# Performance work log

Hardware: AMD Instinct MI355X
Metric: run time of the kernel (lower is better)

Reference implementation:

```python
import jax, jax.numpy as jnp
import numpy as np

ASSET_DIM = 2048
NUM_LATENTS = 32
LATENT_DIM = 64
FLAT_DIM = NUM_LATENTS * LATENT_DIM
SCALE = LATENT_DIM ** (-0.5)


def setup_inputs() -> dict:
    key = jax.random.key(0)
    ks = jax.random.split(key, 7)
    lim = 1.0 / np.sqrt(FLAT_DIM)
    z = jax.random.normal(ks[0], (ASSET_DIM, NUM_LATENTS, LATENT_DIM), dtype=jnp.float32)
    Wq = jax.random.uniform(ks[1], (FLAT_DIM, FLAT_DIM), jnp.float32, -lim, lim)
    bq = jax.random.uniform(ks[2], (FLAT_DIM,), jnp.float32, -lim, lim)
    Wk = jax.random.uniform(ks[3], (FLAT_DIM, FLAT_DIM), jnp.float32, -lim, lim)
    bk = jax.random.uniform(ks[4], (FLAT_DIM,), jnp.float32, -lim, lim)
    Wv = jax.random.uniform(ks[5], (FLAT_DIM, FLAT_DIM), jnp.float32, -lim, lim)
    bv = jax.random.uniform(ks[6], (FLAT_DIM,), jnp.float32, -lim, lim)
    return {"z": z, "Wq": Wq, "bq": bq, "Wk": Wk, "bk": bk, "Wv": Wv, "bv": bv}


def reference(z, Wq, bq, Wk, bk, Wv, bv):
    # z: (A, L, D) -> (A, F) with F = L*D
    zf = z.reshape(ASSET_DIM, FLAT_DIM)
    q = zf @ Wq.T + bq  # (A, F)
    k = zf @ Wk.T + bk  # (A, F)
    v = zf @ Wv.T + bv  # (A, F)
    scores = (q @ k.T) * SCALE          # (A, A)
    attn = jax.nn.softmax(scores, axis=-1)
    # Original does attn[:, :, None] * v[None] then sum over axis 1;
    # that is exactly attn @ v, expressed as a fused matmul here.
    h = attn @ v                        # (A, F)
    return h.reshape(ASSET_DIM, NUM_LATENTS, LATENT_DIM)
```

## Files before the change

### kernel.cpp

```cpp
#include <hip/hip_runtime.h>
#include <hip/hip_bf16.h>


#define AD 2048
#define FD 2048
constexpr float SM_SCALE = 0.125f;

typedef __attribute__((ext_vector_type(8))) short bf16x8;
typedef __attribute__((ext_vector_type(4))) float f32x4;

__device__ __forceinline__ unsigned short f2bf(float f) {
  union { float f; unsigned u; } x; x.f = f;
  unsigned r = x.u + 0x7fffu + ((x.u >> 16) & 1u);
  return (unsigned short)(r >> 16);
}

typedef __attribute__((address_space(1))) const void GVOID;
typedef __attribute__((address_space(3))) void LVOID;

__device__ __forceinline__ void gload16(const void* g, void* l) {
  __builtin_amdgcn_global_load_lds((GVOID*)g, (LVOID*)l, 16, 0, 0);
}

struct GemmArgs {
  const void* A;
  const void* B[3];
  const float* bias[3];
  void* out[3];
  int outmode[3];
  int bf32mask;
  float scale;
};

template<int WROWS, int WCOLS, int MREP, int NREP, int FORCE_MODE, bool MIXEDB, int W2, int NZ>
__global__ __launch_bounds__(WROWS*WCOLS*64, W2) void gemm_d(GemmArgs args) {
  constexpr int NT = WROWS * WCOLS * 64;
  constexpr int BM = WROWS * MREP * 16;
  constexpr int BN = WCOLS * NREP * 16;
  constexpr int SA = BM * 8;
  constexpr int SB = BN * 8;
  static_assert(SA >= NT && SA % NT == 0, "A staging full-coverage");
  static_assert(SB % NT == 0, "B staging full-coverage");

  __shared__ __hip_bfloat16 lA[2][BM * 64];
  __shared__ __hip_bfloat16 lB[2][BN * 64];

  int bnx = blockIdx.x, z;
  if constexpr (NZ > 0) { z = bnx % NZ; bnx /= NZ; }
  else                  { z = blockIdx.z; }
  const int bn = bnx, bm = blockIdx.y;

  const __hip_bfloat16* __restrict__ A = (const __hip_bfloat16*)args.A;
  const __hip_bfloat16* __restrict__ B = (const __hip_bfloat16*)args.B[z];
  const float*          __restrict__ Bf = (const float*)args.B[z];

  const int t    = threadIdx.x;
  const int lane = t & 63;
  const int wv   = t >> 6;
  const int wr   = wv / WCOLS;
  const int wc   = wv % WCOLS;
  const int fr   = lane & 15;
  const int s2   = lane >> 4;

  bool dof32 = false;
  if constexpr (MIXEDB) dof32 = (args.bf32mask >> z) & 1;

  f32x4 acc[MREP][NREP] = {};

  auto scol = [](int s) { return (((s & 7) ^ ((s >> 3) & 7)) * 8); };

  auto STAGE = [&](int k0, int buf) {
    #pragma unroll
    for (int r = 0; r < SA / NT; ++r) {
      const int s = t + r * NT;
      gload16(A + (size_t)(bm * BM + (s >> 3)) * FD + k0 + scol(s), &lA[buf][s * 8]);
    }
    if constexpr (MIXEDB) {
      if (dof32) {
        #pragma unroll
        for (int r = 0; r < SB / NT; ++r) {
          const int s = t + r * NT;
          const float* src = Bf + (size_t)(bn * BN + (s >> 3)) * FD + k0 + scol(s);
          const float4 x = *reinterpret_cast<const float4*>(src);
          const float4 y = *reinterpret_cast<const float4*>(src + 4);
          union { unsigned short us[8]; int4 v; } pk;
          pk.us[0] = f2bf(x.x); pk.us[1] = f2bf(x.y); pk.us[2] = f2bf(x.z); pk.us[3] = f2bf(x.w);
          pk.us[4] = f2bf(y.x); pk.us[5] = f2bf(y.y); pk.us[6] = f2bf(y.z); pk.us[7] = f2bf(y.w);
          *reinterpret_cast<int4*>(&lB[buf][s * 8]) = pk.v;
        }
        return;
      }
    }
    #pragma unroll
    for (int r = 0; r < SB / NT; ++r) {
      const int s = t + r * NT;
      gload16(B + (size_t)(bn * BN + (s >> 3)) * FD + k0 + scol(s), &lB[buf][s * 8]);
    }
  };

  auto COMPUTE = [&](int buf) {
    #pragma unroll
    for (int kk = 0; kk < 2; ++kk) {
      const int ls = s2 + 4 * kk;
      bf16x8 af[MREP], bfr[NREP];
      #pragma unroll
      for (int m = 0; m < MREP; ++m) {
        const int row = wr * (MREP * 16) + m * 16 + fr;
        af[m] = *reinterpret_cast<const bf16x8*>(
            &lA[buf][row * 64 + ((ls ^ (row & 7)) * 8)]);
      }
      #pragma unroll
      for (int n = 0; n < NREP; ++n) {
        const int row = wc * (NREP * 16) + n * 16 + fr;
        bfr[n] = *reinterpret_cast<const bf16x8*>(
            &lB[buf][row * 64 + ((ls ^ (row & 7)) * 8)]);
      }
      #pragma unroll
      for (int m = 0; m < MREP; ++m)
        #pragma unroll
        for (int n = 0; n < NREP; ++n)
          acc[m][n] = __builtin_amdgcn_mfma_f32_16x16x32_bf16(af[m], bfr[n], acc[m][n], 0, 0, 0);
    }
  };

  STAGE(0, 0);
  __syncthreads();
  int cur = 0;
  for (int k0 = 64; k0 < FD; k0 += 64) {
    STAGE(k0, cur ^ 1);
    COMPUTE(cur);
    __syncthreads();
    cur ^= 1;
  }
  COMPUTE(cur);

  const float scale = args.scale;
  const float* __restrict__ bias = args.bias[z];
  const int mode = (FORCE_MODE >= 0) ? FORCE_MODE : args.outmode[z];
  const int row0 = bm * BM + wr * (MREP * 16) + (lane >> 4) * 4;
  const int col0 = bn * BN + wc * (NREP * 16) + fr;

  if (mode == 0) {
    float* __restrict__ out = (float*)args.out[z];
    #pragma unroll
    for (int m = 0; m < MREP; ++m)
      #pragma unroll
      for (int n = 0; n < NREP; ++n) {
        const int cg = col0 + n * 16;
        #pragma unroll
        for (int j = 0; j < 4; ++j)
          out[(size_t)(row0 + m * 16 + j) * FD + cg] = acc[m][n][j] * scale;
      }
  } else if (mode == 1) {
    __hip_bfloat16* __restrict__ out = (__hip_bfloat16*)args.out[z];
    #pragma unroll
    for (int m = 0; m < MREP; ++m)
      #pragma unroll
      for (int n = 0; n < NREP; ++n) {
        const int cg = col0 + n * 16;
        const float badd = bias[cg];
        #pragma unroll
        for (int j = 0; j < 4; ++j) {
          unsigned short b16 = f2bf(acc[m][n][j] + badd);
          out[(size_t)(row0 + m * 16 + j) * FD + cg] = *reinterpret_cast<__hip_bfloat16*>(&b16);
        }
      }
  } else {
    __hip_bfloat16* __restrict__ out = (__hip_bfloat16*)args.out[z];
    #pragma unroll
    for (int m = 0; m < MREP; ++m)
      #pragma unroll
      for (int n = 0; n < NREP; ++n) {
        const int cg = col0 + n * 16;
        const int rg = row0 + m * 16;
        const float badd = bias[cg];
        ushort4 pk;
        pk.x = f2bf(acc[m][n][0] + badd);
        pk.y = f2bf(acc[m][n][1] + badd);
        pk.z = f2bf(acc[m][n][2] + badd);
        pk.w = f2bf(acc[m][n][3] + badd);
        *reinterpret_cast<ushort4*>(out + (size_t)cg * AD + rg) = pk;
      }
  }
}

__global__ __launch_bounds__(256) void cvt_bf16(const float* __restrict__ z,
                                                const float* __restrict__ wq,
                                                const float* __restrict__ wk,
                                                __hip_bfloat16* __restrict__ dst) {
  const size_t NITEM = (size_t)3 * 4096 * 1024 / 8;
  const size_t step = (size_t)gridDim.x * blockDim.x;
  for (size_t idx = (size_t)blockIdx.x * blockDim.x + threadIdx.x; idx < NITEM; idx += step) {
    const int ten = (int)(idx >> 19);
    const size_t off = (idx & ((1u << 19) - 1)) * 8;
    const float* src = (ten == 0) ? z : (ten == 1) ? wq : wk;
    const float4 a = *reinterpret_cast<const float4*>(src + off);
    const float4 b = *reinterpret_cast<const float4*>(src + off + 4);
    union { unsigned short us[8]; int4 v; } pk;
    pk.us[0] = f2bf(a.x); pk.us[1] = f2bf(a.y); pk.us[2] = f2bf(a.z); pk.us[3] = f2bf(a.w);
    pk.us[4] = f2bf(b.x); pk.us[5] = f2bf(b.y); pk.us[6] = f2bf(b.z); pk.us[7] = f2bf(b.w);
    *reinterpret_cast<int4*>(dst + (size_t)ten * 4096 * 1024 + off) = pk.v;
  }
}

__global__ __launch_bounds__(256) void softmax_rows(const float* __restrict__ S,
                                                    __hip_bfloat16* __restrict__ P) {
  const int row = blockIdx.x;
  const int t = threadIdx.x;
  const float* s = S + (size_t)row * AD + t * 8;
  const float4 v0 = *reinterpret_cast<const float4*>(s);
  const float4 v1 = *reinterpret_cast<const float4*>(s + 4);
  float vals[8] = {v0.x, v0.y, v0.z, v0.w, v1.x, v1.y, v1.z, v1.w};

  float m = vals[0];
  #pragma unroll
  for (int j = 1; j < 8; ++j) m = fmaxf(m, vals[j]);
  #pragma unroll
  for (int off = 32; off >= 1; off >>= 1) m = fmaxf(m, __shfl_xor(m, off));

  __shared__ float redm[4], reds[4];
  if ((t & 63) == 0) redm[t >> 6] = m;
  __syncthreads();
  m = fmaxf(fmaxf(redm[0], redm[1]), fmaxf(redm[2], redm[3]));

  float e[8];
  float sum = 0.f;
  #pragma unroll
  for (int j = 0; j < 8; ++j) { e[j] = __expf(vals[j] - m); sum += e[j]; }
  #pragma unroll
  for (int off = 32; off >= 1; off >>= 1) sum += __shfl_xor(sum, off);
  if ((t & 63) == 0) reds[t >> 6] = sum;
  __syncthreads();
  sum = reds[0] + reds[1] + reds[2] + reds[3];
  const float inv = 1.f / sum;

  union { unsigned short us[8]; int4 v; } pk;
  #pragma unroll
  for (int j = 0; j < 8; ++j) pk.us[j] = f2bf(e[j] * inv);
  *reinterpret_cast<int4*>(P + (size_t)row * AD + t * 8) = pk.v;
}

extern "C" void kernel_launch(void* const* d_in, const int* in_sizes, int n_in,
                              void* d_out, int out_size, void* d_ws, size_t ws_size,
                              hipStream_t stream) {
  const float* z  = (const float*)d_in[0];
  const float* Wq = (const float*)d_in[1];
  const float* bq = (const float*)d_in[2];
  const float* Wk = (const float*)d_in[3];
  const float* bk = (const float*)d_in[4];
  const float* Wv = (const float*)d_in[5];
  const float* bv = (const float*)d_in[6];

  char* ws = (char*)d_ws;
  const size_t MB8 = (size_t)8 * 1024 * 1024;
  __hip_bfloat16* zb  = (__hip_bfloat16*)(ws);
  __hip_bfloat16* Wqb = (__hip_bfloat16*)(ws + MB8);
  __hip_bfloat16* Wkb = (__hip_bfloat16*)(ws + 2*MB8);
  __hip_bfloat16* vT  = (__hip_bfloat16*)(ws + 3*MB8);
  float*          S   = (float*)(ws);
  __hip_bfloat16* P   = (__hip_bfloat16*)(ws + 2*MB8);
  __hip_bfloat16* qb  = (__hip_bfloat16*)d_out;
  __hip_bfloat16* kb  = (__hip_bfloat16*)d_out + (size_t)AD * FD;

  cvt_bf16<<<dim3(2048), dim3(256), 0, stream>>>(z, Wq, Wk, (__hip_bfloat16*)ws);

  {
    GemmArgs a;
    a.A = zb;
    a.B[0] = Wqb; a.B[1] = Wkb; a.B[2] = Wv;
    a.bias[0] = bq; a.bias[1] = bk; a.bias[2] = bv;
    a.out[0] = qb; a.out[1] = kb; a.out[2] = vT;
    a.outmode[0] = 1; a.outmode[1] = 1; a.outmode[2] = 2;
    a.bf32mask = 0b100;
    a.scale = 1.0f;
    gemm_d<2, 4, 4, 2, -1, true, 2, 0>
        <<<dim3(AD/128, AD/128, 3), dim3(512), 0, stream>>>(a);
  }
  {
    GemmArgs a = {};
    a.A = qb;
    a.B[0] = kb;
    a.bias[0] = nullptr;
    a.out[0] = S;
    a.outmode[0] = 0;
    a.bf32mask = 0;
    a.scale = SM_SCALE;
    gemm_d<4, 2, 2, 2, 0, false, 2, 0><<<dim3(AD/64, AD/128, 1), dim3(512), 0, stream>>>(a);
  }
  softmax_rows<<<dim3(AD), dim3(256), 0, stream>>>(S, P);
  {
    GemmArgs a = {};
    a.A = P;
    a.B[0] = vT;
    a.bias[0] = nullptr;
    a.out[0] = d_out;
    a.outmode[0] = 0;
    a.bf32mask = 0;
    a.scale = 1.0f;
    gemm_d<4, 2, 2, 2, 0, false, 2, 0><<<dim3(AD/64, AD/128, 1), dim3(512), 0, stream>>>(a);
  }
}
```

Measured before the change: 152.3 us.

## Pre-convert Wv to bf16 and split V projection into separate GEMM launch

Wv is now converted to bf16 in the conversion pre-pass, so the V projection can use async global-to-LDS loads instead of in-loop fp32 loads with per-element conversion. The QK projection and V projection become separate launches, each with compile-time output mode, which removes the runtime mode and mixed-B branches. The V GEMM uses a smaller 64x128 tile. In exchange this adds one kernel launch and an extra full read and write of Wv in the conversion kernel, and the workspace buffers are reassigned to fit the new Wv buffer.

```diff
diff --git a/kernel.cpp b/kernel.cpp
--- a/kernel.cpp
+++ b/kernel.cpp
@@ -24,15 +24,13 @@
 
 struct GemmArgs {
   const void* A;
-  const void* B[3];
-  const float* bias[3];
-  void* out[3];
-  int outmode[3];
-  int bf32mask;
+  const void* B[2];
+  const float* bias[2];
+  void* out[2];
   float scale;
 };
 
-template<int WROWS, int WCOLS, int MREP, int NREP, int FORCE_MODE, bool MIXEDB, int W2, int NZ>
+template<int WROWS, int WCOLS, int MREP, int NREP, int MODE, int W2>
 __global__ __launch_bounds__(WROWS*WCOLS*64, W2) void gemm_d(GemmArgs args) {
   constexpr int NT = WROWS * WCOLS * 64;
   constexpr int BM = WROWS * MREP * 16;
@@ -45,14 +43,11 @@
   __shared__ __hip_bfloat16 lA[2][BM * 64];
   __shared__ __hip_bfloat16 lB[2][BN * 64];
 
-  int bnx = blockIdx.x, z;
-  if constexpr (NZ > 0) { z = bnx % NZ; bnx /= NZ; }
-  else                  { z = blockIdx.z; }
-  const int bn = bnx, bm = blockIdx.y;
+  const int z  = blockIdx.z;
+  const int bn = blockIdx.x, bm = blockIdx.y;
 
   const __hip_bfloat16* __restrict__ A = (const __hip_bfloat16*)args.A;
   const __hip_bfloat16* __restrict__ B = (const __hip_bfloat16*)args.B[z];
-  const float*          __restrict__ Bf = (const float*)args.B[z];
 
   const int t    = threadIdx.x;
   const int lane = t & 63;
@@ -62,9 +57,6 @@
   const int fr   = lane & 15;
   const int s2   = lane >> 4;
 
-  bool dof32 = false;
-  if constexpr (MIXEDB) dof32 = (args.bf32mask >> z) & 1;
-
   f32x4 acc[MREP][NREP] = {};
 
   auto scol = [](int s) { return (((s & 7) ^ ((s >> 3) & 7)) * 8); };
@@ -74,22 +66,6 @@
     for (int r = 0; r < SA / NT; ++r) {
       const int s = t + r * NT;
       gload16(A + (size_t)(bm * BM + (s >> 3)) * FD + k0 + scol(s), &lA[buf][s * 8]);
-    }
-    if constexpr (MIXEDB) {
-      if (dof32) {
-        #pragma unroll
-        for (int r = 0; r < SB / NT; ++r) {
-          const int s = t + r * NT;
-          const float* src = Bf + (size_t)(bn * BN + (s >> 3)) * FD + k0 + scol(s);
-          const float4 x = *reinterpret_cast<const float4*>(src);
-          const float4 y = *reinterpret_cast<const float4*>(src + 4);
-          union { unsigned short us[8]; int4 v; } pk;
-          pk.us[0] = f2bf(x.x); pk.us[1] = f2bf(x.y); pk.us[2] = f2bf(x.z); pk.us[3] = f2bf(x.w);
-          pk.us[4] = f2bf(y.x); pk.us[5] = f2bf(y.y); pk.us[6] = f2bf(y.z); pk.us[7] = f2bf(y.w);
-          *reinterpret_cast<int4*>(&lB[buf][s * 8]) = pk.v;
-        }
-        return;
-      }
     }
     #pragma unroll
     for (int r = 0; r < SB / NT; ++r) {
@@ -136,11 +112,10 @@
 
   const float scale = args.scale;
   const float* __restrict__ bias = args.bias[z];
-  const int mode = (FORCE_MODE >= 0) ? FORCE_MODE : args.outmode[z];
   const int row0 = bm * BM + wr * (MREP * 16) + (lane >> 4) * 4;
   const int col0 = bn * BN + wc * (NREP * 16) + fr;
 
-  if (mode == 0) {
+  if constexpr (MODE == 0) {
     float* __restrict__ out = (float*)args.out[z];
     #pragma unroll
     for (int m = 0; m < MREP; ++m)
@@ -151,7 +126,7 @@
         for (int j = 0; j < 4; ++j)
           out[(size_t)(row0 + m * 16 + j) * FD + cg] = acc[m][n][j] * scale;
       }
-  } else if (mode == 1) {
+  } else if constexpr (MODE == 1) {
     __hip_bfloat16* __restrict__ out = (__hip_bfloat16*)args.out[z];
     #pragma unroll
     for (int m = 0; m < MREP; ++m)
@@ -187,13 +162,14 @@
 __global__ __launch_bounds__(256) void cvt_bf16(const float* __restrict__ z,
                                                 const float* __restrict__ wq,
                                                 const float* __restrict__ wk,
+                                                const float* __restrict__ wv,
                                                 __hip_bfloat16* __restrict__ dst) {
-  const size_t NITEM = (size_t)3 * 4096 * 1024 / 8;
+  const size_t NITEM = (size_t)4 * 4096 * 1024 / 8;
   const size_t step = (size_t)gridDim.x * blockDim.x;
   for (size_t idx = (size_t)blockIdx.x * blockDim.x + threadIdx.x; idx < NITEM; idx += step) {
     const int ten = (int)(idx >> 19);
     const size_t off = (idx & ((1u << 19) - 1)) * 8;
-    const float* src = (ten == 0) ? z : (ten == 1) ? wq : wk;
+    const float* src = (ten == 0) ? z : (ten == 1) ? wq : (ten == 2) ? wk : wv;
     const float4 a = *reinterpret_cast<const float4*>(src + off);
     const float4 b = *reinterpret_cast<const float4*>(src + off + 4);
     union { unsigned short us[8]; int4 v; } pk;
@@ -256,25 +232,32 @@
   __hip_bfloat16* zb  = (__hip_bfloat16*)(ws);
   __hip_bfloat16* Wqb = (__hip_bfloat16*)(ws + MB8);
   __hip_bfloat16* Wkb = (__hip_bfloat16*)(ws + 2*MB8);
-  __hip_bfloat16* vT  = (__hip_bfloat16*)(ws + 3*MB8);
-  float*          S   = (float*)(ws);
-  __hip_bfloat16* P   = (__hip_bfloat16*)(ws + 2*MB8);
+  __hip_bfloat16* Wvb = (__hip_bfloat16*)(ws + 3*MB8);
+  __hip_bfloat16* vT  = (__hip_bfloat16*)(ws + MB8);
+  float*          S   = (float*)(ws + 2*MB8);
+  __hip_bfloat16* P   = (__hip_bfloat16*)(ws);
   __hip_bfloat16* qb  = (__hip_bfloat16*)d_out;
   __hip_bfloat16* kb  = (__hip_bfloat16*)d_out + (size_t)AD * FD;
 
-  cvt_bf16<<<dim3(2048), dim3(256), 0, stream>>>(z, Wq, Wk, (__hip_bfloat16*)ws);
+  cvt_bf16<<<dim3(2048), dim3(256), 0, stream>>>(z, Wq, Wk, Wv, (__hip_bfloat16*)ws);
 
   {
     GemmArgs a;
     a.A = zb;
-    a.B[0] = Wqb; a.B[1] = Wkb; a.B[2] = Wv;
-    a.bias[0] = bq; a.bias[1] = bk; a.bias[2] = bv;
-    a.out[0] = qb; a.out[1] = kb; a.out[2] = vT;
-    a.outmode[0] = 1; a.outmode[1] = 1; a.outmode[2] = 2;
-    a.bf32mask = 0b100;
+    a.B[0] = Wqb;  a.B[1] = Wkb;
+    a.bias[0] = bq; a.bias[1] = bk;
+    a.out[0] = qb;  a.out[1] = kb;
     a.scale = 1.0f;
-    gemm_d<2, 4, 4, 2, -1, true, 2, 0>
-        <<<dim3(AD/128, AD/128, 3), dim3(512), 0, stream>>>(a);
+    gemm_d<2, 4, 4, 2, 1, 2><<<dim3(AD/128, AD/128, 2), dim3(512), 0, stream>>>(a);
+  }
+  {
+    GemmArgs a = {};
+    a.A = zb;
+    a.B[0] = Wvb;
+    a.bias[0] = bv;
+    a.out[0] = vT;
+    a.scale = 1.0f;
+    gemm_d<4, 2, 2, 2, 2, 2><<<dim3(AD/64, AD/128, 1), dim3(512), 0, stream>>>(a);
   }
   {
     GemmArgs a = {};
@@ -282,10 +265,8 @@
     a.B[0] = kb;
     a.bias[0] = nullptr;
     a.out[0] = S;
-    a.outmode[0] = 0;
-    a.bf32mask = 0;
     a.scale = SM_SCALE;
-    gemm_d<4, 2, 2, 2, 0, false, 2, 0><<<dim3(AD/64, AD/128, 1), dim3(512), 0, stream>>>(a);
+    gemm_d<4, 2, 2, 2, 0, 2><<<dim3(AD/64, AD/128, 1), dim3(512), 0, stream>>>(a);
   }
   softmax_rows<<<dim3(AD), dim3(256), 0, stream>>>(S, P);
   {
@@ -294,9 +275,7 @@
     a.B[0] = vT;
     a.bias[0] = nullptr;
     a.out[0] = d_out;
-    a.outmode[0] = 0;
-    a.bf32mask = 0;
     a.scale = 1.0f;
-    gemm_d<4, 2, 2, 2, 0, false, 2, 0><<<dim3(AD/64, AD/128, 1), dim3(512), 0, stream>>>(a);
-  }
-}
+    gemm_d<4, 2, 2, 2, 0, 2><<<dim3(AD/64, AD/128, 1), dim3(512), 0, stream>>>(a);
+  }
+}
```

New measurement: 141.2 us. -7.3%, faster.
